# Optimization experiments

Hardware: AMD Instinct MI355X
Metric: run time of the kernel (lower is better)

## Reference

```python
import jax, jax.numpy as jnp
import numpy as np

B, H, W, C = 16, 56, 56, 256
NH, WS, SS = 8, 7, 3            # heads, window size, shift size
N = WS * WS                     # tokens per window (49)
NW = (H // WS) * (W // WS)      # windows per image (64)
HID = 4 * C                     # mlp hidden
SCALE = (C // NH) ** -0.5
EPS = 1e-5


def _rel_pos_index():
    coords = np.stack(np.meshgrid(np.arange(WS), np.arange(WS), indexing='ij'))  # (2,WS,WS)
    cf = coords.reshape(2, -1)
    rel = (cf[:, :, None] - cf[:, None, :]).transpose(1, 2, 0).copy()  # (N,N,2)
    rel[:, :, 0] += WS - 1
    rel[:, :, 1] += WS - 1
    rel[:, :, 0] *= 2 * WS - 1
    return rel.sum(-1).reshape(-1)  # (N*N,)

REL_IDX = jnp.asarray(_rel_pos_index())


def _attn_mask():
    # Swin SW-MSA mask for the cyclic shift
    img = np.zeros((H, W), np.float32)
    cnt = 0
    for hs in (slice(0, -WS), slice(-WS, -SS), slice(-SS, None)):
        for ws_ in (slice(0, -WS), slice(-WS, -SS), slice(-SS, None)):
            img[hs, ws_] = cnt
            cnt += 1
    mw = img.reshape(H // WS, WS, W // WS, WS).transpose(0, 2, 1, 3).reshape(-1, N)
    am = mw[:, None, :] - mw[:, :, None]
    return np.where(am != 0, -100.0, 0.0).astype(np.float32)  # (NW,N,N)


def layernorm(x, g, b):
    mu = x.mean(-1, keepdims=True)
    var = jnp.mean((x - mu) ** 2, axis=-1, keepdims=True)
    return (x - mu) * jax.lax.rsqrt(var + EPS) * g + b


def window_partition(x):  # (B,H,W,C) -> (B*NW,N,C)
    b = x.shape[0]
    x = x.reshape(b, H // WS, WS, W // WS, WS, C).transpose(0, 1, 3, 2, 4, 5)
    return x.reshape(-1, N, C)


def window_reverse(w):  # (B*NW,N,C) -> (B,H,W,C)
    x = w.reshape(-1, H // WS, W // WS, WS, WS, C).transpose(0, 1, 3, 2, 4, 5)
    return x.reshape(-1, H, W, C)


def setup_inputs() -> dict:
    key = jax.random.key(0)
    ks = jax.random.split(key, 16)
    sd = 0.02
    return {
        'x': jax.random.normal(ks[0], (B, H * W, C), jnp.float32),
        'w_qkv': jax.random.normal(ks[1], (C, 3 * C), jnp.float32) * sd,
        'b_qkv': jnp.zeros((3 * C,), jnp.float32),
        'rel_bias': jax.random.normal(ks[2], ((2 * WS - 1) ** 2, NH), jnp.float32) * sd,
        'w_proj': jax.random.normal(ks[3], (C, C), jnp.float32) * sd,
        'b_proj': jnp.zeros((C,), jnp.float32),
        'g1': jnp.ones((C,), jnp.float32),
        'beta1': jnp.zeros((C,), jnp.float32),
        'g2': jnp.ones((C,), jnp.float32),
        'beta2': jnp.zeros((C,), jnp.float32),
        'w_fc1': jax.random.normal(ks[4], (C, HID), jnp.float32) * sd,
        'b_fc1': jnp.zeros((HID,), jnp.float32),
        'w_fc2': jax.random.normal(ks[5], (HID, C), jnp.float32) * sd,
        'b_fc2': jnp.zeros((C,), jnp.float32),
        'attn_mask': jnp.asarray(_attn_mask()),
    }


def reference(x, w_qkv, b_qkv, rel_bias, w_proj, b_proj, g1, beta1, g2, beta2,
              w_fc1, b_fc1, w_fc2, b_fc2, attn_mask):
    shortcut = x
    xn = layernorm(x, g1, beta1).reshape(B, H, W, C)
    # cyclic shift (shift_size > 0 path)
    xs = jnp.roll(xn, shift=(-SS, -SS), axis=(1, 2))
    xw = window_partition(xs)                                   # (B*NW, N, C)
    qkv = (xw @ w_qkv + b_qkv).reshape(-1, N, 3, NH, C // NH)
    q, k, v = [jnp.transpose(qkv[:, :, i], (0, 2, 1, 3)) for i in range(3)]  # (Bw,NH,N,hd)
    attn = jnp.einsum('whnd,whmd->whnm', q * SCALE, k)          # (Bw,NH,N,N)
    rpb = rel_bias[REL_IDX].reshape(N, N, NH).transpose(2, 0, 1)  # (NH,N,N)
    attn = attn + rpb[None]
    attn = attn.reshape(B, NW, NH, N, N) + attn_mask[None, :, None]
    attn = jax.nn.softmax(attn.reshape(-1, NH, N, N), axis=-1)
    out = jnp.einsum('whnm,whmd->whnd', attn, v)                # (Bw,NH,N,hd)
    out = out.transpose(0, 2, 1, 3).reshape(-1, N, C)
    out = out @ w_proj + b_proj
    xs = window_reverse(out)                                    # (B,H,W,C)
    xr = jnp.roll(xs, shift=(SS, SS), axis=(1, 2)).reshape(B, H * W, C)
    x = shortcut + xr
    h = layernorm(x, g2, beta2)
    h = jax.nn.gelu(h @ w_fc1 + b_fc1, approximate=False) @ w_fc2 + b_fc2
    return x + h
```

## Files before the change

kernel.cpp:

```cpp
#include <hip/hip_runtime.h>
#include <hip/hip_bf16.h>

typedef unsigned short u16;
typedef __bf16 bf16x8 __attribute__((ext_vector_type(8)));
typedef float f32x4 __attribute__((ext_vector_type(4)));
typedef unsigned int u32x4 __attribute__((ext_vector_type(4)));

#define SCALE_F 0.17677669529663687f

__device__ __forceinline__ u16 f2b(float f) {
    unsigned u = __builtin_bit_cast(unsigned, f);
    u = (u + 0x7fffu + ((u >> 16) & 1u)) >> 16;
    return (u16)u;
}
__device__ __forceinline__ float b2f(u16 b) {
    unsigned u = ((unsigned)b) << 16;
    return __builtin_bit_cast(float, u);
}

__device__ __forceinline__ f32x4 mfma16(bf16x8 a, bf16x8 b, f32x4 c) {
    return __builtin_amdgcn_mfma_f32_16x16x32_bf16(a, b, c, 0, 0, 0);
}

__global__ __launch_bounds__(256)
void prep_kernel(const float* __restrict__ wqkv, const float* __restrict__ wproj,
                 const float* __restrict__ wfc1, const float* __restrict__ wfc2,
                 const float* __restrict__ relb, const float* __restrict__ amask,
                 u16* __restrict__ wqkvT, u16* __restrict__ wprojT,
                 u16* __restrict__ wfc1T, u16* __restrict__ wfc2T,
                 float* __restrict__ bm)
{
    int idx = blockIdx.x * 256 + threadIdx.x;
    if (idx < 196608) { int n = idx >> 8, k = idx & 255; wqkvT[idx] = f2b(wqkv[k*768 + n]); return; }
    idx -= 196608;
    if (idx < 65536)  { int n = idx >> 8, k = idx & 255; wprojT[idx] = f2b(wproj[k*256 + n]); return; }
    idx -= 65536;
    if (idx < 262144) { int n = idx >> 8, k = idx & 255; wfc1T[idx] = f2b(wfc1[k*1024 + n]); return; }
    idx -= 262144;
    if (idx < 262144) { int n = idx >> 10, k = idx & 1023; wfc2T[idx] = f2b(wfc2[k*256 + n]); return; }
    idx -= 262144;
    int m = idx & 63, t = idx >> 6;
    int n = t & 63; t >>= 6;
    int h = t & 7;  t >>= 3;
    float v = -1e30f;
    if (n < 49 && m < 49) {
        int iq = n / 7, jq = n - iq * 7, ik = m / 7, jk = m - ik * 7;
        int rel = (iq - ik + 6) * 13 + (jq - jk + 6);
        v = relb[rel * 8 + h] + amask[(t * 49 + n) * 49 + m];
    }
    bm[idx] = v;
}

__global__ __launch_bounds__(256)
void ln_kernel(const float* __restrict__ x, const u16* __restrict__ xb,
               const float* __restrict__ g, const float* __restrict__ be,
               u16* __restrict__ out, const int mode)
{
    const int wid  = ((blockIdx.x << 8) + threadIdx.x) >> 6;
    const int lane = threadIdx.x & 63;
    float4 v;
    if (mode == 0) {
        int bw = wid / 49, nt = wid - bw * 49;
        int b = bw >> 6, widx = bw & 63;
        int wh = widx >> 3, ww = widx & 7;
        int ti = nt / 7, tj = nt - ti * 7;
        int hh = wh * 7 + ti + 3; if (hh >= 56) hh -= 56;
        int wp = ww * 7 + tj + 3; if (wp >= 56) wp -= 56;
        size_t srcoff = ((size_t)b * 3136 + hh * 56 + wp) << 8;
        v = *(const float4*)(x + srcoff + (lane << 2));
    } else {
        ushort4 raw = *(const ushort4*)(xb + ((size_t)wid << 8) + (lane << 2));
        v.x = b2f(raw.x); v.y = b2f(raw.y); v.z = b2f(raw.z); v.w = b2f(raw.w);
    }
    float s  = v.x + v.y + v.z + v.w;
    float s2 = fmaf(v.x, v.x, fmaf(v.y, v.y, fmaf(v.z, v.z, v.w * v.w)));
    #pragma unroll
    for (int k = 1; k < 64; k <<= 1) { s += __shfl_xor(s, k); s2 += __shfl_xor(s2, k); }
    const float mu   = s * 0.00390625f;
    const float rstd = rsqrtf(s2 * 0.00390625f - mu * mu + 1e-5f);
    float4 gv = *(const float4*)(g  + (lane << 2));
    float4 bv = *(const float4*)(be + (lane << 2));
    ushort4 o;
    o.x = f2b((v.x - mu) * rstd * gv.x + bv.x);
    o.y = f2b((v.y - mu) * rstd * gv.y + bv.y);
    o.z = f2b((v.z - mu) * rstd * gv.z + bv.z);
    o.w = f2b((v.w - mu) * rstd * gv.w + bv.w);
    *(ushort4*)(out + ((size_t)wid << 8) + (lane << 2)) = o;
}

template<int MODE>
__global__ __launch_bounds__(256)
void gemm128(const u16* __restrict__ A, const u16* __restrict__ Bt,
             const float* __restrict__ bias, void* __restrict__ Cout,
             const int N, const int K, const void* __restrict__ resid,
             const int NB)
{
    constexpr int LDA = 40;
    __shared__ __align__(16) u16 As[128 * LDA];
    __shared__ __align__(16) u16 Bs[128 * LDA];

    const int tid  = threadIdx.x;
    const int wave = tid >> 6, lane = tid & 63;
    const int q = lane >> 4, l15 = lane & 15;
    const int wm = wave >> 1, wn = wave & 1;

    const int bid  = blockIdx.x;
    const int xcd  = bid & 7;
    const int t    = bid >> 3;
    const int colb = t % NB;
    const int rowb = xcd + ((t / NB) << 3);
    const int m0 = rowb << 7, n0 = colb << 7;

    f32x4 acc[4][4] = {};

    const int ar = tid >> 2;
    const int ac = (tid & 3) << 3;
    const u16* Ag = A  + (size_t)(m0 + ar) * K + ac;
    const u16* Bg = Bt + (size_t)(n0 + ar) * K + ac;
    const size_t rstep = (size_t)64 * K;

    u32x4 ra0 = *(const u32x4*)Ag;
    u32x4 ra1 = *(const u32x4*)(Ag + rstep);
    u32x4 rb0 = *(const u32x4*)Bg;
    u32x4 rb1 = *(const u32x4*)(Bg + rstep);

    const int KT = K >> 5;
    for (int kt = 0; kt < KT; ++kt) {
        __syncthreads();
        *(u32x4*)&As[ar * LDA + ac]        = ra0;
        *(u32x4*)&As[(ar + 64) * LDA + ac] = ra1;
        *(u32x4*)&Bs[ar * LDA + ac]        = rb0;
        *(u32x4*)&Bs[(ar + 64) * LDA + ac] = rb1;
        if (kt + 1 < KT) {
            const u16* Ag2 = Ag + (kt + 1) * 32;
            const u16* Bg2 = Bg + (kt + 1) * 32;
            ra0 = *(const u32x4*)Ag2;
            ra1 = *(const u32x4*)(Ag2 + rstep);
            rb0 = *(const u32x4*)Bg2;
            rb1 = *(const u32x4*)(Bg2 + rstep);
        }
        __syncthreads();
        bf16x8 af[4], bfv[4];
        #pragma unroll
        for (int i = 0; i < 4; ++i)
            af[i] = *(const bf16x8*)&As[(wm * 64 + i * 16 + l15) * LDA + q * 8];
        #pragma unroll
        for (int j = 0; j < 4; ++j)
            bfv[j] = *(const bf16x8*)&Bs[(wn * 64 + j * 16 + l15) * LDA + q * 8];
        #pragma unroll
        for (int i = 0; i < 4; ++i)
            #pragma unroll
            for (int j = 0; j < 4; ++j)
                acc[i][j] = mfma16(af[i], bfv[j], acc[i][j]);
    }

    #pragma unroll
    for (int i = 0; i < 4; ++i) {
        #pragma unroll
        for (int r = 0; r < 4; ++r) {
            const int m = m0 + wm * 64 + i * 16 + q * 4 + r;
            size_t dstrow = 0;
            if (MODE == 1) {
                int bw = m / 49, nt = m - bw * 49;
                int b = bw >> 6, widx = bw & 63;
                int wh = widx >> 3, ww2 = widx & 7;
                int ti = nt / 7, tj = nt - ti * 7;
                int hh = wh * 7 + ti + 3;  if (hh >= 56) hh -= 56;
                int wp = ww2 * 7 + tj + 3; if (wp >= 56) wp -= 56;
                dstrow = ((size_t)b * 3136 + hh * 56 + wp) << 8;
            }
            #pragma unroll
            for (int j = 0; j < 4; ++j) {
                const int col = n0 + wn * 64 + j * 16 + l15;
                float v = acc[i][j][r] + bias[col];
                if (MODE == 0) {
                    ((u16*)Cout)[(size_t)m * N + col] = f2b(v);
                } else if (MODE == 2) {
                    float y = 0.7978845608028654f * (v + 0.044715f * v * v * v);
                    float tt = __expf(2.0f * y);
                    float rr = __builtin_amdgcn_rcpf(tt + 1.0f);
                    v = v - v * rr;
                    ((u16*)Cout)[(size_t)m * N + col] = f2b(v);
                } else if (MODE == 3) {
                    const size_t o = (size_t)m * N + col;
                    ((float*)Cout)[o] = b2f(((const u16*)resid)[o]) + v;
                } else {
                    const size_t o = dstrow + col;
                    ((u16*)Cout)[o] = f2b(((const float*)resid)[o] + v);
                }
            }
        }
    }
}

__global__ __launch_bounds__(64)
void attn_kernel(const u16* __restrict__ qkv, const float* __restrict__ bm,
                 u16* __restrict__ out)
{
    constexpr int LDP = 72;
    __shared__ __align__(16) u16 Pl[64 * LDP];
    __shared__ __align__(16) u16 Vt[32 * LDP];

    const int bw   = blockIdx.x >> 3;
    const int h    = blockIdx.x & 7;
    const int widx = bw & 63;
    const int lane = threadIdx.x;
    const int q = lane >> 4, l15 = lane & 15;

    const u16* base = qkv + (size_t)bw * 49 * 768 + h * 32;

    {
        const int key = lane;
        const u16* vp = base + 512 + (size_t)(key < 49 ? key : 0) * 768;
        __align__(16) u16 tmp[32];
        #pragma unroll
        for (int c = 0; c < 4; ++c)
            *(u32x4*)&tmp[c * 8] = *(const u32x4*)(vp + c * 8);
        #pragma unroll
        for (int d = 0; d < 32; ++d)
            Vt[d * LDP + key] = (key < 49) ? tmp[d] : (u16)0;
    }

    bf16x8 aq[4], bk[4];
    #pragma unroll
    for (int i = 0; i < 4; ++i) {
        int row = i * 16 + l15; row = (row < 49) ? row : 0;
        aq[i] = *(const bf16x8*)(base + (size_t)row * 768 + q * 8);
    }
    #pragma unroll
    for (int j = 0; j < 4; ++j) {
        int key = j * 16 + l15; key = (key < 49) ? key : 0;
        bk[j] = *(const bf16x8*)(base + (size_t)key * 768 + 256 + q * 8);
    }
    f32x4 s[4][4];
    #pragma unroll
    for (int i = 0; i < 4; ++i)
        #pragma unroll
        for (int j = 0; j < 4; ++j) {
            f32x4 z = {0.f, 0.f, 0.f, 0.f};
            s[i][j] = mfma16(aq[i], bk[j], z);
        }

    const float* bmb = bm + ((size_t)(widx * 8 + h) << 12);
    #pragma unroll
    for (int i = 0; i < 4; ++i) {
        #pragma unroll
        for (int r = 0; r < 4; ++r) {
            const int n = i * 16 + q * 4 + r;
            const float* rowp = bmb + (n << 6) + l15;
            #pragma unroll
            for (int j = 0; j < 4; ++j)
                s[i][j][r] = fmaf(s[i][j][r], SCALE_F, rowp[j * 16]);
        }
    }

    #pragma unroll
    for (int i = 0; i < 4; ++i) {
        #pragma unroll
        for (int r = 0; r < 4; ++r) {
            float mx = fmaxf(fmaxf(s[i][0][r], s[i][1][r]), fmaxf(s[i][2][r], s[i][3][r]));
            #pragma unroll
            for (int k = 1; k < 16; k <<= 1) mx = fmaxf(mx, __shfl_xor(mx, k));
            float p[4], sum = 0.f;
            #pragma unroll
            for (int j = 0; j < 4; ++j) { p[j] = __expf(s[i][j][r] - mx); sum += p[j]; }
            #pragma unroll
            for (int k = 1; k < 16; k <<= 1) sum += __shfl_xor(sum, k);
            const float inv = 1.0f / sum;
            const int n = i * 16 + q * 4 + r;
            #pragma unroll
            for (int j = 0; j < 4; ++j)
                Pl[n * LDP + j * 16 + l15] = f2b(p[j] * inv);
        }
    }
    __syncthreads();

    f32x4 o[4][2] = {};
    #pragma unroll
    for (int ks = 0; ks < 2; ++ks) {
        bf16x8 ap[4], bv[2];
        #pragma unroll
        for (int i = 0; i < 4; ++i)
            ap[i] = *(const bf16x8*)&Pl[(i * 16 + l15) * LDP + ks * 32 + q * 8];
        #pragma unroll
        for (int jd = 0; jd < 2; ++jd)
            bv[jd] = *(const bf16x8*)&Vt[(jd * 16 + l15) * LDP + ks * 32 + q * 8];
        #pragma unroll
        for (int i = 0; i < 4; ++i)
            #pragma unroll
            for (int jd = 0; jd < 2; ++jd)
                o[i][jd] = mfma16(ap[i], bv[jd], o[i][jd]);
    }

    #pragma unroll
    for (int i = 0; i < 4; ++i) {
        #pragma unroll
        for (int r = 0; r < 4; ++r) {
            const int n = i * 16 + q * 4 + r;
            if (n < 49) {
                u16* op = out + ((size_t)(bw * 49 + n) << 8) + h * 32;
                #pragma unroll
                for (int jd = 0; jd < 2; ++jd)
                    op[jd * 16 + l15] = f2b(o[i][jd][r]);
            }
        }
    }
}

extern "C" void kernel_launch(void* const* d_in, const int* in_sizes, int n_in,
                              void* d_out, int out_size, void* d_ws, size_t ws_size,
                              hipStream_t stream) {
    const float* x      = (const float*)d_in[0];
    const float* w_qkv  = (const float*)d_in[1];
    const float* b_qkv  = (const float*)d_in[2];
    const float* rel_b  = (const float*)d_in[3];
    const float* w_proj = (const float*)d_in[4];
    const float* b_proj = (const float*)d_in[5];
    const float* g1     = (const float*)d_in[6];
    const float* be1    = (const float*)d_in[7];
    const float* g2     = (const float*)d_in[8];
    const float* be2    = (const float*)d_in[9];
    const float* w_fc1  = (const float*)d_in[10];
    const float* b_fc1  = (const float*)d_in[11];
    const float* w_fc2  = (const float*)d_in[12];
    const float* b_fc2  = (const float*)d_in[13];
    const float* amask  = (const float*)d_in[14];

    char* ws = (char*)d_ws;
    u16*   xw     = (u16*)(ws);
    u16*   qkvb   = (u16*)(ws + 25690112);
    u16*   attno  = (u16*)(ws + 102760448);
    u16*   x2b    = (u16*)(ws + 128450560);
    u16*   wqkvT  = (u16*)(ws + 154140672);
    u16*   wprojT = (u16*)(ws + 154533888);
    u16*   wfc1T  = (u16*)(ws + 154664960);
    u16*   wfc2T  = (u16*)(ws + 155189248);
    float* bm     = (float*)(ws + 155713536);
    u16*   h1     = qkvb;

    prep_kernel<<<12288, 256, 0, stream>>>(w_qkv, w_proj, w_fc1, w_fc2, rel_b, amask,
                                           wqkvT, wprojT, wfc1T, wfc2T, bm);
    ln_kernel<<<12544, 256, 0, stream>>>(x, nullptr, g1, be1, xw, 0);
    gemm128<0><<<392 * 6, 256, 0, stream>>>(xw, wqkvT, b_qkv, qkvb, 768, 256, nullptr, 6);
    attn_kernel<<<8192, 64, 0, stream>>>(qkvb, bm, attno);
    gemm128<1><<<392 * 2, 256, 0, stream>>>(attno, wprojT, b_proj, x2b, 256, 256, x, 2);
    ln_kernel<<<12544, 256, 0, stream>>>(nullptr, x2b, g2, be2, xw, 2);
    gemm128<2><<<392 * 8, 256, 0, stream>>>(xw, wfc1T, b_fc1, h1, 1024, 256, nullptr, 8);
    gemm128<3><<<392 * 2, 256, 0, stream>>>(h1, wfc2T, b_fc2, (float*)d_out, 256, 1024, x2b, 2);
}
```

Measured before the change: 348.4 us.

## Use direct global-to-LDS loads with double-buffered shared tiles in GEMM

The GEMM mainloop now fills shared memory with global_load_lds (buffer loads that bypass registers) instead of loading into registers and then storing to LDS. The LDS tile is double buffered and rearranged into k-chunk-major order. The next tile's loads are issued before the current tile's MFMAs, and only one barrier per iteration remains. This removes register staging and a sync, but depends on the asynchronous LDS loads being complete when the barrier is reached, and the new layout may cause bank conflicts.

```diff
diff --git a/kernel.cpp b/kernel.cpp
--- a/kernel.cpp
+++ b/kernel.cpp
@@ -20,6 +20,12 @@
 
 __device__ __forceinline__ f32x4 mfma16(bf16x8 a, bf16x8 b, f32x4 c) {
     return __builtin_amdgcn_mfma_f32_16x16x32_bf16(a, b, c, 0, 0, 0);
+}
+
+__device__ __forceinline__ void gload16(const u16* g, u16* l) {
+    __builtin_amdgcn_global_load_lds(
+        (const __attribute__((address_space(1))) void*)g,
+        (__attribute__((address_space(3))) void*)l, 16, 0, 0);
 }
 
 __global__ __launch_bounds__(256)
@@ -95,9 +101,8 @@
              const int N, const int K, const void* __restrict__ resid,
              const int NB)
 {
-    constexpr int LDA = 40;
-    __shared__ __align__(16) u16 As[128 * LDA];
-    __shared__ __align__(16) u16 Bs[128 * LDA];
+    __shared__ __align__(16) u16 As[2][4 * 128 * 8];
+    __shared__ __align__(16) u16 Bs[2][4 * 128 * 8];
 
     const int tid  = threadIdx.x;
     const int wave = tid >> 6, lane = tid & 63;
@@ -113,45 +118,40 @@
 
     f32x4 acc[4][4] = {};
 
-    const int ar = tid >> 2;
-    const int ac = (tid & 3) << 3;
-    const u16* Ag = A  + (size_t)(m0 + ar) * K + ac;
-    const u16* Bg = Bt + (size_t)(n0 + ar) * K + ac;
-    const size_t rstep = (size_t)64 * K;
-
-    u32x4 ra0 = *(const u32x4*)Ag;
-    u32x4 ra1 = *(const u32x4*)(Ag + rstep);
-    u32x4 rb0 = *(const u32x4*)Bg;
-    u32x4 rb1 = *(const u32x4*)(Bg + rstep);
+    const u16* Ag = A  + (size_t)(m0 + lane) * K + wave * 8;
+    const u16* Bg = Bt + (size_t)(n0 + lane) * K + wave * 8;
+    const size_t half = (size_t)64 * K;
+
+    gload16(Ag,        &As[0][(wave * 128 +  0) * 8]);
+    gload16(Ag + half, &As[0][(wave * 128 + 64) * 8]);
+    gload16(Bg,        &Bs[0][(wave * 128 +  0) * 8]);
+    gload16(Bg + half, &Bs[0][(wave * 128 + 64) * 8]);
+    __syncthreads();
 
     const int KT = K >> 5;
     for (int kt = 0; kt < KT; ++kt) {
-        __syncthreads();
-        *(u32x4*)&As[ar * LDA + ac]        = ra0;
-        *(u32x4*)&As[(ar + 64) * LDA + ac] = ra1;
-        *(u32x4*)&Bs[ar * LDA + ac]        = rb0;
-        *(u32x4*)&Bs[(ar + 64) * LDA + ac] = rb1;
+        const int cur = kt & 1, nxt = cur ^ 1;
         if (kt + 1 < KT) {
             const u16* Ag2 = Ag + (kt + 1) * 32;
             const u16* Bg2 = Bg + (kt + 1) * 32;
-            ra0 = *(const u32x4*)Ag2;
-            ra1 = *(const u32x4*)(Ag2 + rstep);
-            rb0 = *(const u32x4*)Bg2;
-            rb1 = *(const u32x4*)(Bg2 + rstep);
-        }
-        __syncthreads();
+            gload16(Ag2,        &As[nxt][(wave * 128 +  0) * 8]);
+            gload16(Ag2 + half, &As[nxt][(wave * 128 + 64) * 8]);
+            gload16(Bg2,        &Bs[nxt][(wave * 128 +  0) * 8]);
+            gload16(Bg2 + half, &Bs[nxt][(wave * 128 + 64) * 8]);
+        }
         bf16x8 af[4], bfv[4];
         #pragma unroll
         for (int i = 0; i < 4; ++i)
-            af[i] = *(const bf16x8*)&As[(wm * 64 + i * 16 + l15) * LDA + q * 8];
+            af[i] = *(const bf16x8*)&As[cur][(q * 128 + wm * 64 + i * 16 + l15) * 8];
         #pragma unroll
         for (int j = 0; j < 4; ++j)
-            bfv[j] = *(const bf16x8*)&Bs[(wn * 64 + j * 16 + l15) * LDA + q * 8];
+            bfv[j] = *(const bf16x8*)&Bs[cur][(q * 128 + wn * 64 + j * 16 + l15) * 8];
         #pragma unroll
         for (int i = 0; i < 4; ++i)
             #pragma unroll
             for (int j = 0; j < 4; ++j)
                 acc[i][j] = mfma16(af[i], bfv[j], acc[i][j]);
+        __syncthreads();
     }
 
     #pragma unroll
```

After: 404.3 us. +16.0%, slower.
